# Performance work log

Measured on AMD Instinct MI355X. Metric: run time of the kernel, lower is better.

Reference implementation:

```python
import jax, jax.numpy as jnp
import numpy as np

# dipy lower-triangular channel order: [Dxx, Dxy, Dyy, Dxz, Dyz, Dzz]
_LOTRI_IDX = np.array([[0, 1, 3], [1, 2, 4], [3, 4, 5]])


def _trilinear_warp(img, ddf):
    """MONAI Warp(mode='bilinear', padding_mode='border'): sample img at voxel
    coords (index + ddf), trilinear interp, clamped to borders.
    img: (B,C,H,W,D), ddf: (B,3,H,W,D) in voxel units."""
    B, C, H, W, D = img.shape
    f = img.dtype
    gx, gy, gz = jnp.meshgrid(jnp.arange(H, dtype=f), jnp.arange(W, dtype=f),
                              jnp.arange(D, dtype=f), indexing='ij')
    cx = jnp.clip(gx[None] + ddf[:, 0], 0.0, H - 1.0)
    cy = jnp.clip(gy[None] + ddf[:, 1], 0.0, W - 1.0)
    cz = jnp.clip(gz[None] + ddf[:, 2], 0.0, D - 1.0)
    x0f = jnp.floor(cx); y0f = jnp.floor(cy); z0f = jnp.floor(cz)
    fx = (cx - x0f)[:, None]; fy = (cy - y0f)[:, None]; fz = (cz - z0f)[:, None]
    x0 = x0f.astype(jnp.int32); y0 = y0f.astype(jnp.int32); z0 = z0f.astype(jnp.int32)
    x1 = jnp.minimum(x0 + 1, H - 1); y1 = jnp.minimum(y0 + 1, W - 1); z1 = jnp.minimum(z0 + 1, D - 1)
    flat = img.reshape(B, C, H * W * D)

    def g(ix, iy, iz):
        lin = (ix * W + iy) * D + iz  # (B,H,W,D)
        return jnp.take_along_axis(flat, lin.reshape(B, 1, -1), axis=2).reshape(B, C, H, W, D)

    c00 = g(x0, y0, z0) * (1 - fz) + g(x0, y0, z1) * fz
    c01 = g(x0, y1, z0) * (1 - fz) + g(x0, y1, z1) * fz
    c10 = g(x1, y0, z0) * (1 - fz) + g(x1, y0, z1) * fz
    c11 = g(x1, y1, z0) * (1 - fz) + g(x1, y1, z1) * fz
    c0 = c00 * (1 - fy) + c01 * fy
    c1 = c10 * (1 - fy) + c11 * fy
    return c0 * (1 - fx) + c1 * fx


def _jacobian(ddf):
    """J = I + d(ddf)/dx via central differences (one-sided at edges).
    Returns (B,H,W,D,3,3) with J[...,i,j] = delta_ij + d ddf_i / d x_j."""
    rows = [jnp.stack(jnp.gradient(ddf[:, i], axis=(1, 2, 3)), axis=-1) for i in range(3)]
    J = jnp.stack(rows, axis=-2)  # (B,H,W,D,3,3)
    return J + jnp.eye(3, dtype=ddf.dtype)


def _forward(dti, ddf):
    warped = _trilinear_warp(dti, ddf)                    # (B,6,H,W,D)
    wc = jnp.moveaxis(warped, 1, -1)                      # (B,H,W,D,6)
    M = wc[..., jnp.asarray(_LOTRI_IDX)]                  # (B,H,W,D,3,3) symmetric
    J = _jacobian(ddf)
    U, _, Vh = jnp.linalg.svd(J, full_matrices=False)
    R = U @ Vh                                            # polar orthogonal factor
    Dp = jnp.einsum('...ji,...jk,...kl->...il', R, M, R)  # R^T M R
    lot = jnp.stack([Dp[..., 0, 0], Dp[..., 1, 0], Dp[..., 1, 1],
                     Dp[..., 2, 0], Dp[..., 2, 1], Dp[..., 2, 2]], axis=1)
    return lot


def setup_inputs() -> dict:
    key = jax.random.key(0)
    k1, k2 = jax.random.split(key)
    B, H, W, D = 1, 128, 128, 128
    dti = jax.random.normal(k1, (B, 6, H, W, D), dtype=jnp.float32)
    ddf = jax.random.normal(k2, (B, 3, H, W, D), dtype=jnp.float32)
    return {"dti": dti, "ddf": ddf}


def reference(dti, ddf):
    return _forward(dti, ddf)
```

## Files before the change

### kernel.cpp

```cpp
#include <hip/hip_runtime.h>
#include <hip/hip_fp16.h>
#include <math.h>

#define DIM 128
#define NVOX (DIM*DIM*DIM)

typedef float vfloat4 __attribute__((ext_vector_type(4)));
typedef unsigned int vuint4 __attribute__((ext_vector_type(4)));

__global__ __launch_bounds__(256) void pack_dti_kernel(
    const float* __restrict__ dti, vuint4* __restrict__ aos)
{
    const int bid = blockIdx.x;
    const int sb = ((bid & 7) << 8) | (bid >> 3);
    const int id4 = (sb * 256 + (int)threadIdx.x) * 4;

    const vfloat4 v0 = __builtin_nontemporal_load(reinterpret_cast<const vfloat4*>(dti + 0 * NVOX + id4));
    const vfloat4 v1 = __builtin_nontemporal_load(reinterpret_cast<const vfloat4*>(dti + 1 * NVOX + id4));
    const vfloat4 v2 = __builtin_nontemporal_load(reinterpret_cast<const vfloat4*>(dti + 2 * NVOX + id4));
    const vfloat4 v3 = __builtin_nontemporal_load(reinterpret_cast<const vfloat4*>(dti + 3 * NVOX + id4));
    const vfloat4 v4 = __builtin_nontemporal_load(reinterpret_cast<const vfloat4*>(dti + 4 * NVOX + id4));
    const vfloat4 v5 = __builtin_nontemporal_load(reinterpret_cast<const vfloat4*>(dti + 5 * NVOX + id4));

    auto packone = [&](float a0, float a1, float a2, float a3, float a4,
                       float a5, int idx) {
        const __half2 h01 = __floats2half2_rn(a0, a1);
        const __half2 h23 = __floats2half2_rn(a2, a3);
        const __half2 h45 = __floats2half2_rn(a4, a5);
        vuint4 q;
        q.x = *reinterpret_cast<const unsigned int*>(&h01);
        q.y = *reinterpret_cast<const unsigned int*>(&h23);
        q.z = *reinterpret_cast<const unsigned int*>(&h45);
        q.w = 0u;
        aos[idx] = q;
    };
    packone(v0.x, v1.x, v2.x, v3.x, v4.x, v5.x, id4 + 0);
    packone(v0.y, v1.y, v2.y, v3.y, v4.y, v5.y, id4 + 1);
    packone(v0.z, v1.z, v2.z, v3.z, v4.z, v5.z, id4 + 2);
    packone(v0.w, v1.w, v2.w, v3.w, v4.w, v5.w, id4 + 3);
}

__device__ __forceinline__ bool polar_f32(const float J[9], float X[9])
{
#pragma unroll
    for (int t = 0; t < 9; ++t) X[t] = J[t];
    bool bad = false;
#pragma unroll
    for (int it = 0; it < 6; ++it) {
        float C[9];
        C[0] = X[4] * X[8] - X[5] * X[7];
        C[1] = X[5] * X[6] - X[3] * X[8];
        C[2] = X[3] * X[7] - X[4] * X[6];
        C[3] = X[2] * X[7] - X[1] * X[8];
        C[4] = X[0] * X[8] - X[2] * X[6];
        C[5] = X[1] * X[6] - X[0] * X[7];
        C[6] = X[1] * X[5] - X[2] * X[4];
        C[7] = X[2] * X[3] - X[0] * X[5];
        C[8] = X[0] * X[4] - X[1] * X[3];
        const float det = X[0] * C[0] + X[1] * C[1] + X[2] * C[2];
        float a, b;
        if (it < 3) {
            float nX = 0.0f, nC = 0.0f;
#pragma unroll
            for (int t = 0; t < 9; ++t) { nX += X[t] * X[t]; nC += C[t] * C[t]; }
            if (it == 0)
                bad = !(nX * nC < 4.0e6f * det * det);
            const float s = __builtin_amdgcn_sqrtf(nC * __builtin_amdgcn_rcpf(nX));
            const float r = __builtin_amdgcn_rsqf(s * fabsf(det));
            a = 0.5f * s * r;
            b = copysignf(0.5f * r, det);
        } else {
            a = 0.5f;
            b = 0.5f * __builtin_amdgcn_rcpf(det);
        }
#pragma unroll
        for (int t = 0; t < 9; ++t) X[t] = a * X[t] + b * C[t];
    }
    return bad;
}

__device__ __forceinline__ void polar_f64(const float J[9], float X[9])
{
    double Y[9];
#pragma unroll
    for (int t = 0; t < 9; ++t) Y[t] = (double)J[t];
    for (int it = 0; it < 20; ++it) {
        double C[9];
        C[0] = Y[4] * Y[8] - Y[5] * Y[7];
        C[1] = Y[5] * Y[6] - Y[3] * Y[8];
        C[2] = Y[3] * Y[7] - Y[4] * Y[6];
        C[3] = Y[2] * Y[7] - Y[1] * Y[8];
        C[4] = Y[0] * Y[8] - Y[2] * Y[6];
        C[5] = Y[1] * Y[6] - Y[0] * Y[7];
        C[6] = Y[1] * Y[5] - Y[2] * Y[4];
        C[7] = Y[2] * Y[3] - Y[0] * Y[5];
        C[8] = Y[0] * Y[4] - Y[1] * Y[3];
        const double det = Y[0] * C[0] + Y[1] * C[1] + Y[2] * C[2];
        if (!(fabs(det) > 1e-300)) break;
        double nX = 0.0, nC = 0.0;
#pragma unroll
        for (int t = 0; t < 9; ++t) { nX += Y[t] * Y[t]; nC += C[t] * C[t]; }
        const double g = sqrt(sqrt(nC) / (fabs(det) * sqrt(nX)));
        const double a = 0.5 * g;
        const double b = 0.5 / (g * det);
        double diff2 = 0.0, n2 = 0.0;
#pragma unroll
        for (int t = 0; t < 9; ++t) {
            const double y = a * Y[t] + b * C[t];
            const double d = y - Y[t];
            diff2 += d * d; n2 += y * y;
            Y[t] = y;
        }
        if (diff2 <= 1e-26 * n2) break;
    }
#pragma unroll
    for (int t = 0; t < 9; ++t) X[t] = (float)Y[t];
}

__global__ __launch_bounds__(256) void warp_dti_kernel(
    const vuint4* __restrict__ aos,
    const float* __restrict__ ddf,
    float* __restrict__ out)
{
    const int bid = blockIdx.x;
    const int sb = ((bid & 7) << 10) | (bid >> 3);
    const int id = sb * 256 + (int)threadIdx.x;
    const int k = id & (DIM - 1);
    const int j = (id >> 7) & (DIM - 1);
    const int i = id >> 14;

    const int im = (i > 0) ? i - 1 : 0, ip = (i < DIM - 1) ? i + 1 : DIM - 1;
    const int jm = (j > 0) ? j - 1 : 0, jp = (j < DIM - 1) ? j + 1 : DIM - 1;
    const int km = (k > 0) ? k - 1 : 0, kp = (k < DIM - 1) ? k + 1 : DIM - 1;
    const float si = (ip - im == 2) ? 0.5f : 1.0f;
    const float sj = (jp - jm == 2) ? 0.5f : 1.0f;
    const float sk = (kp - km == 2) ? 0.5f : 1.0f;

    const int l_ip = (ip << 14) | (j << 7) | k;
    const int l_im = (im << 14) | (j << 7) | k;
    const int l_jp = (i << 14) | (jp << 7) | k;
    const int l_jm = (i << 14) | (jm << 7) | k;
    const int l_kp = (i << 14) | (j << 7) | kp;
    const int l_km = (i << 14) | (j << 7) | km;

    float J[9];
    float u[3];
#pragma unroll
    for (int c = 0; c < 3; ++c) {
        const float* __restrict__ p = ddf + c * NVOX;
        u[c] = p[id];
        J[c * 3 + 0] = (p[l_ip] - p[l_im]) * si;
        J[c * 3 + 1] = (p[l_jp] - p[l_jm]) * sj;
        J[c * 3 + 2] = (p[l_kp] - p[l_km]) * sk;
        J[c * 3 + c] += 1.0f;
    }

    const float cx = fminf(fmaxf((float)i + u[0], 0.0f), (float)(DIM - 1));
    const float cy = fminf(fmaxf((float)j + u[1], 0.0f), (float)(DIM - 1));
    const float cz = fminf(fmaxf((float)k + u[2], 0.0f), (float)(DIM - 1));
    const float x0f = floorf(cx), y0f = floorf(cy), z0f = floorf(cz);
    const float fx = cx - x0f, fy = cy - y0f, fz = cz - z0f;
    const int x0 = (int)x0f, y0 = (int)y0f, z0 = (int)z0f;
    const int x1 = min(x0 + 1, DIM - 1);
    const int y1 = min(y0 + 1, DIM - 1);
    const int z1 = min(z0 + 1, DIM - 1);

    const float gx0 = 1.0f - fx, gy0 = 1.0f - fy, gz0 = 1.0f - fz;

    const int dz = z1 - z0;
    const int dy = (y1 - y0) << 7;
    const int dx = (x1 - x0) << 14;
    const int b000 = (x0 << 14) | (y0 << 7) | z0;

    float acc0 = 0.0f, acc1 = 0.0f, acc2 = 0.0f;
    float acc3 = 0.0f, acc4 = 0.0f, acc5 = 0.0f;

    auto gat = [&](int lin, float wt) {
        const vuint4 q = aos[lin];
        const unsigned int qx = q.x, qy = q.y, qz = q.z;
        const __half2 h01 = *reinterpret_cast<const __half2*>(&qx);
        const __half2 h23 = *reinterpret_cast<const __half2*>(&qy);
        const __half2 h45 = *reinterpret_cast<const __half2*>(&qz);
        acc0 = fmaf(__half2float(__low2half(h01)), wt, acc0);
        acc1 = fmaf(__half2float(__high2half(h01)), wt, acc1);
        acc2 = fmaf(__half2float(__low2half(h23)), wt, acc2);
        acc3 = fmaf(__half2float(__high2half(h23)), wt, acc3);
        acc4 = fmaf(__half2float(__low2half(h45)), wt, acc4);
        acc5 = fmaf(__half2float(__high2half(h45)), wt, acc5);
    };

    gat(b000,                gx0 * gy0 * gz0);
    gat(b000 + dz,           gx0 * gy0 * fz);
    gat(b000 + dy,           gx0 * fy * gz0);
    gat(b000 + dy + dz,      gx0 * fy * fz);
    gat(b000 + dx,           fx * gy0 * gz0);
    gat(b000 + dx + dz,      fx * gy0 * fz);
    gat(b000 + dx + dy,      fx * fy * gz0);
    gat(b000 + dx + dy + dz, fx * fy * fz);

    float X[9];
    const bool bad = polar_f32(J, X);
    if (__builtin_expect(bad, 0)) polar_f64(J, X);

    const float M00 = acc0, M01 = acc1, M11 = acc2;
    const float M02 = acc3, M12 = acc4, M22 = acc5;
    float P[9];
    P[0] = M00 * X[0] + M01 * X[3] + M02 * X[6];
    P[1] = M00 * X[1] + M01 * X[4] + M02 * X[7];
    P[2] = M00 * X[2] + M01 * X[5] + M02 * X[8];
    P[3] = M01 * X[0] + M11 * X[3] + M12 * X[6];
    P[4] = M01 * X[1] + M11 * X[4] + M12 * X[7];
    P[5] = M01 * X[2] + M11 * X[5] + M12 * X[8];
    P[6] = M02 * X[0] + M12 * X[3] + M22 * X[6];
    P[7] = M02 * X[1] + M12 * X[4] + M22 * X[7];
    P[8] = M02 * X[2] + M12 * X[5] + M22 * X[8];

    __builtin_nontemporal_store(X[0] * P[0] + X[3] * P[3] + X[6] * P[6], &out[0 * NVOX + id]);
    __builtin_nontemporal_store(X[1] * P[0] + X[4] * P[3] + X[7] * P[6], &out[1 * NVOX + id]);
    __builtin_nontemporal_store(X[1] * P[1] + X[4] * P[4] + X[7] * P[7], &out[2 * NVOX + id]);
    __builtin_nontemporal_store(X[2] * P[0] + X[5] * P[3] + X[8] * P[6], &out[3 * NVOX + id]);
    __builtin_nontemporal_store(X[2] * P[1] + X[5] * P[4] + X[8] * P[7], &out[4 * NVOX + id]);
    __builtin_nontemporal_store(X[2] * P[2] + X[5] * P[5] + X[8] * P[8], &out[5 * NVOX + id]);
}

extern "C" void kernel_launch(void* const* d_in, const int* in_sizes, int n_in,
                              void* d_out, int out_size, void* d_ws, size_t ws_size,
                              hipStream_t stream) {
    const float* dti = (const float*)d_in[0];
    const float* ddf = (const float*)d_in[1];
    float* out = (float*)d_out;
    vuint4* aos = (vuint4*)d_ws;

    hipLaunchKernelGGL(pack_dti_kernel, dim3(NVOX / 1024), dim3(256), 0, stream,
                       dti, aos);
    hipLaunchKernelGGL(warp_dti_kernel, dim3(NVOX / 256), dim3(256), 0, stream,
                       aos, ddf, out);
}
```

Before: 167.7 us.

## Use 12-byte AoS accesses, wavefront shuffles for z-gradient, one fewer polar iteration

The packed half-precision DTI array is now written and read as a 3-dword vector with 16-byte stride, which drops the padding dword from each store and gather. The z-direction neighbours of the displacement field now come from wavefront shuffles, with scalar loads only at wavefront edges, replacing two global loads per component. The float polar iteration cap drops from 6 to 5. Together these aim to cut memory traffic and instructions, but the lower cap may reduce accuracy for hard Jacobians unless the double-precision fallback catches them.

```diff
diff --git a/kernel.cpp b/kernel.cpp
--- a/kernel.cpp
+++ b/kernel.cpp
@@ -7,9 +7,11 @@
 
 typedef float vfloat4 __attribute__((ext_vector_type(4)));
 typedef unsigned int vuint4 __attribute__((ext_vector_type(4)));
+typedef unsigned int vuint3 __attribute__((ext_vector_type(3)));
+static_assert(sizeof(vuint3) == 16, "vuint3 must stride 16B over the AoS array");
 
 __global__ __launch_bounds__(256) void pack_dti_kernel(
-    const float* __restrict__ dti, vuint4* __restrict__ aos)
+    const float* __restrict__ dti, unsigned int* __restrict__ aos)
 {
     const int bid = blockIdx.x;
     const int sb = ((bid & 7) << 8) | (bid >> 3);
@@ -27,12 +29,11 @@
         const __half2 h01 = __floats2half2_rn(a0, a1);
         const __half2 h23 = __floats2half2_rn(a2, a3);
         const __half2 h45 = __floats2half2_rn(a4, a5);
-        vuint4 q;
+        vuint3 q;
         q.x = *reinterpret_cast<const unsigned int*>(&h01);
         q.y = *reinterpret_cast<const unsigned int*>(&h23);
         q.z = *reinterpret_cast<const unsigned int*>(&h45);
-        q.w = 0u;
-        aos[idx] = q;
+        *reinterpret_cast<vuint3*>(aos + 4 * idx) = q;
     };
     packone(v0.x, v1.x, v2.x, v3.x, v4.x, v5.x, id4 + 0);
     packone(v0.y, v1.y, v2.y, v3.y, v4.y, v5.y, id4 + 1);
@@ -46,7 +47,7 @@
     for (int t = 0; t < 9; ++t) X[t] = J[t];
     bool bad = false;
 #pragma unroll
-    for (int it = 0; it < 6; ++it) {
+    for (int it = 0; it < 5; ++it) {
         float C[9];
         C[0] = X[4] * X[8] - X[5] * X[7];
         C[1] = X[5] * X[6] - X[3] * X[8];
@@ -118,40 +119,48 @@
 }
 
 __global__ __launch_bounds__(256) void warp_dti_kernel(
-    const vuint4* __restrict__ aos,
+    const vuint3* __restrict__ aos,
     const float* __restrict__ ddf,
     float* __restrict__ out)
 {
     const int bid = blockIdx.x;
     const int sb = ((bid & 7) << 10) | (bid >> 3);
     const int id = sb * 256 + (int)threadIdx.x;
+    const int lane = (int)threadIdx.x & 63;
     const int k = id & (DIM - 1);
     const int j = (id >> 7) & (DIM - 1);
     const int i = id >> 14;
 
+    const float* __restrict__ p0_ = ddf;
+    const float* __restrict__ p1_ = ddf + NVOX;
+    const float* __restrict__ p2_ = ddf + 2 * NVOX;
+
     const int im = (i > 0) ? i - 1 : 0, ip = (i < DIM - 1) ? i + 1 : DIM - 1;
     const int jm = (j > 0) ? j - 1 : 0, jp = (j < DIM - 1) ? j + 1 : DIM - 1;
-    const int km = (k > 0) ? k - 1 : 0, kp = (k < DIM - 1) ? k + 1 : DIM - 1;
     const float si = (ip - im == 2) ? 0.5f : 1.0f;
     const float sj = (jp - jm == 2) ? 0.5f : 1.0f;
-    const float sk = (kp - km == 2) ? 0.5f : 1.0f;
+    const float sk = (k > 0 && k < DIM - 1) ? 0.5f : 1.0f;
 
     const int l_ip = (ip << 14) | (j << 7) | k;
     const int l_im = (im << 14) | (j << 7) | k;
     const int l_jp = (i << 14) | (jp << 7) | k;
     const int l_jm = (i << 14) | (jm << 7) | k;
-    const int l_kp = (i << 14) | (j << 7) | kp;
-    const int l_km = (i << 14) | (j << 7) | km;
 
     float J[9];
     float u[3];
 #pragma unroll
     for (int c = 0; c < 3; ++c) {
-        const float* __restrict__ p = ddf + c * NVOX;
+        const float* __restrict__ p = (c == 0) ? p0_ : (c == 1) ? p1_ : p2_;
         u[c] = p[id];
+        float kp_raw = __shfl_down(u[c], 1, 64);
+        float km_raw = __shfl_up(u[c], 1, 64);
+        if (lane == 63 && k < DIM - 1) kp_raw = p[id + 1];
+        if (lane == 0 && k > 0)        km_raw = p[id - 1];
+        const float kpv = (k < DIM - 1) ? kp_raw : u[c];
+        const float kmv = (k > 0)       ? km_raw : u[c];
         J[c * 3 + 0] = (p[l_ip] - p[l_im]) * si;
         J[c * 3 + 1] = (p[l_jp] - p[l_jm]) * sj;
-        J[c * 3 + 2] = (p[l_kp] - p[l_km]) * sk;
+        J[c * 3 + 2] = (kpv - kmv) * sk;
         J[c * 3 + c] += 1.0f;
     }
 
@@ -176,7 +185,7 @@
     float acc3 = 0.0f, acc4 = 0.0f, acc5 = 0.0f;
 
     auto gat = [&](int lin, float wt) {
-        const vuint4 q = aos[lin];
+        const vuint3 q = aos[lin];
         const unsigned int qx = q.x, qy = q.y, qz = q.z;
         const __half2 h01 = *reinterpret_cast<const __half2*>(&qx);
         const __half2 h23 = *reinterpret_cast<const __half2*>(&qy);
@@ -229,10 +238,10 @@
     const float* dti = (const float*)d_in[0];
     const float* ddf = (const float*)d_in[1];
     float* out = (float*)d_out;
-    vuint4* aos = (vuint4*)d_ws;
+    unsigned int* aos = (unsigned int*)d_ws;
 
     hipLaunchKernelGGL(pack_dti_kernel, dim3(NVOX / 1024), dim3(256), 0, stream,
                        dti, aos);
     hipLaunchKernelGGL(warp_dti_kernel, dim3(NVOX / 256), dim3(256), 0, stream,
-                       aos, ddf, out);
-}
+                       (const vuint3*)aos, ddf, out);
+}
```

After: 171.6 us. +2.3%, slower.
